# Optimization experiments

Hardware: AMD Instinct MI355X
Metric: run time of the kernel (lower is better)

Reference implementation:

```python
import jax, jax.numpy as jnp
import numpy as np

B, S, D = 2, 2048, 2048
H = 16
KV_RANK = 512
NOPE, ROPE = 128, 64
QK_HD = NOPE + ROPE  # 192
V_HD = 128
SCALE = QK_HD ** -0.5
EPS = 1.1920929e-07  # torch RMSNorm default eps = finfo(fp32).eps
NEG = -1e9


def rmsnorm(x, w):
    return x * jax.lax.rsqrt(jnp.mean(x * x, axis=-1, keepdims=True) + EPS) * w


def apply_rope(x, freqs):
    # x: (b, s, h, r) interleaved pairs; freqs: (s, r//2) angles
    sh = x.shape
    xr = x.reshape(*sh[:-1], -1, 2)
    a, b = xr[..., 0], xr[..., 1]
    cos = jnp.cos(freqs)[None, :, None, :]
    sin = jnp.sin(freqs)[None, :, None, :]
    return jnp.stack([a * cos - b * sin, a * sin + b * cos], axis=-1).reshape(sh)


def setup_inputs() -> dict:
    key = jax.random.key(0)
    ks = jax.random.split(key, 8)
    inv = lambda k, shape, fan_in: jax.random.uniform(k, shape, jnp.float32, -1.0, 1.0) / np.sqrt(fan_in)
    x = jax.random.normal(ks[0], (B, S, D), jnp.float32)
    freqs = jax.random.uniform(ks[1], (S, ROPE // 2), jnp.float32) * np.float32(np.pi)
    mask = jnp.where(jnp.triu(jnp.ones((S, S), bool), k=1), jnp.float32(NEG), jnp.float32(0.0))
    wq_w = inv(ks[2], (H * QK_HD, D), D)
    wq_b = jnp.zeros((H * QK_HD,), jnp.float32)
    wkv_a_w = inv(ks[3], (KV_RANK + ROPE, D), D)
    wkv_a_b = jnp.zeros((KV_RANK + ROPE,), jnp.float32)
    kv_norm_w = jnp.ones((KV_RANK,), jnp.float32)
    wkv_b_w = inv(ks[4], (H * (NOPE + V_HD), KV_RANK), KV_RANK)
    wo_w = inv(ks[5], (D, H * V_HD), H * V_HD)
    wo_b = jnp.zeros((D,), jnp.float32)
    return dict(x=x, freqs=freqs, mask=mask, wq_w=wq_w, wq_b=wq_b,
                wkv_a_w=wkv_a_w, wkv_a_b=wkv_a_b, kv_norm_w=kv_norm_w,
                wkv_b_w=wkv_b_w, wo_w=wo_w, wo_b=wo_b)


def reference(x, freqs, mask, wq_w, wq_b, wkv_a_w, wkv_a_b, kv_norm_w, wkv_b_w, wo_w, wo_b):
    b, s, _ = x.shape
    # q projection (q_lora_rank == 0 path)
    q = (x @ wq_w.T + wq_b).reshape(b, s, H, QK_HD)
    q_nope, q_pe = q[..., :NOPE], q[..., NOPE:]
    q_pe = apply_rope(q_pe, freqs)
    # latent kv projection
    kv = x @ wkv_a_w.T + wkv_a_b
    kv, k_pe = kv[..., :KV_RANK], kv[..., KV_RANK:]
    k_pe = apply_rope(k_pe[:, :, None, :], freqs)[:, :, 0, :]  # (b, t, r)
    kv_proj = rmsnorm(kv, kv_norm_w)  # (b, t, c)
    wkv_b = wkv_b_w.reshape(H, NOPE + V_HD, KV_RANK)
    # absorb K-nope projection into q
    q_nope = jnp.einsum('bshd,hdc->bshc', q_nope, wkv_b[:, :NOPE])
    scores = (jnp.einsum('bshc,btc->bsht', q_nope, kv_proj)
              + jnp.einsum('bshr,btr->bsht', q_pe, k_pe)) * SCALE
    scores = scores + mask[None, :, None, :]
    scores = jax.nn.softmax(scores.astype(jnp.float32), axis=-1).astype(x.dtype)
    out = jnp.einsum('bsht,btc->bshc', scores, kv_proj)
    out = jnp.einsum('bshc,hdc->bshd', out, wkv_b[:, -V_HD:])
    return out.reshape(b, s, H * V_HD) @ wo_w.T + wo_b
```

## Files before the change

kernel.cpp:

```cpp
#include <hip/hip_runtime.h>
#include <hip/hip_bf16.h>
#include <math.h>

#define B_ 2
#define S_ 2048
#define H_ 16
#define SCALE_ 0.07216878364870323f
#define SL2_ (0.07216878364870323f * 1.4426950408889634f)
#define EPS_ 1.1920929e-07f
#define M0_ 8.0f

typedef __attribute__((ext_vector_type(8))) short bf16x8;
typedef __attribute__((ext_vector_type(4))) float f32x4;
union U4 { uint4 u; bf16x8 v; f32x4 f; };

__device__ __forceinline__ uint bfbits(float x) {
    uint u = __float_as_uint(x);
    return (u + 0x7fffu + ((u >> 16) & 1u)) >> 16;
}
__device__ __forceinline__ uint pack2bf(float a, float b) {
    return bfbits(a) | (bfbits(b) << 16);
}
__device__ __forceinline__ uint cvtpk(float a, float b) {
    uint r;
    asm("v_cvt_pk_bf16_f32 %0, %1, %2" : "=v"(r) : "v"(a), "v"(b));
    return r;
}
__device__ __forceinline__ void gld_lds16(const ushort* g, ushort* l) {
    __builtin_amdgcn_global_load_lds(
        (const __attribute__((address_space(1))) uint*)g,
        (__attribute__((address_space(3))) uint*)l, 16, 0, 0);
}

template<bool OUT_BF16>
__global__ __launch_bounds__(256) void mgemm(
    const ushort* __restrict__ A, int lda, long long aOff1, long long aOff2,
    const ushort* __restrict__ Bm, int ldb, long long bOff1, long long bOff2,
    const float* __restrict__ bias, float scale,
    void* __restrict__ Cv, int ldc, long long cOff1, long long cOff2,
    int K, int zDiv)
{
    __shared__ ushort As[128 * 32];
    __shared__ ushort Bs[128 * 32];

    const int z = blockIdx.z;
    const int z1 = z % zDiv, z2 = z / zDiv;
    A  += z1 * aOff1 + z2 * aOff2;
    Bm += z1 * bOff1 + z2 * bOff2;
    const long long cBase = z1 * cOff1 + z2 * cOff2;

    const int n0 = blockIdx.x * 128;
    const int m0 = blockIdx.y * 128;
    const int tid = threadIdx.x;
    const int w   = tid >> 6;
    const int l   = tid & 63;
    const int m   = l & 15;
    const int q4  = l >> 4;
    const int mw  = (w & 1) * 64;
    const int nw  = (w >> 1) * 64;
    const int sr  = l >> 2;
    const int sc  = l & 3;

    f32x4 acc[4][4];
#pragma unroll
    for (int i = 0; i < 4; ++i)
#pragma unroll
        for (int j = 0; j < 4; ++j) acc[i][j] = (f32x4){0.f, 0.f, 0.f, 0.f};

    for (int k0 = 0; k0 < K; k0 += 32) {
#pragma unroll
        for (int jj = 0; jj < 2; ++jj) {
            const int slot = w * 2 + jj;
            const int row  = slot * 16 + sr;
            const int g    = sc ^ ((row >> 1) & 3);
            gld_lds16(&A[(long long)(m0 + row) * lda + k0 + g * 8], &As[slot * 512]);
            gld_lds16(&Bm[(long long)(n0 + row) * ldb + k0 + g * 8], &Bs[slot * 512]);
        }
        __syncthreads();

        U4 af[4], bf[4];
#pragma unroll
        for (int i = 0; i < 4; ++i) {
            const int ra = mw + i * 16 + m;
            af[i].u = *(const uint4*)&As[ra * 32 + (q4 ^ ((ra >> 1) & 3)) * 8];
            const int rb = nw + i * 16 + m;
            bf[i].u = *(const uint4*)&Bs[rb * 32 + (q4 ^ ((rb >> 1) & 3)) * 8];
        }
#pragma unroll
        for (int i = 0; i < 4; ++i)
#pragma unroll
            for (int j = 0; j < 4; ++j)
                acc[i][j] = __builtin_amdgcn_mfma_f32_16x16x32_bf16(
                    af[i].v, bf[j].v, acc[i][j], 0, 0, 0);
        __syncthreads();
    }

#pragma unroll
    for (int j = 0; j < 4; ++j) {
        const int cn = n0 + nw + j * 16 + m;
        const float bv = bias ? bias[cn] : 0.0f;
#pragma unroll
        for (int i = 0; i < 4; ++i) {
            const int rw = m0 + mw + i * 16 + q4 * 4;
#pragma unroll
            for (int r = 0; r < 4; ++r) {
                const float val = acc[i][j][r] * scale + bv;
                if (OUT_BF16)
                    ((ushort*)Cv)[cBase + (long long)(rw + r) * ldc + cn] =
                        (ushort)bfbits(val);
                else
                    ((float*)Cv)[cBase + (long long)(rw + r) * ldc + cn] = val;
            }
        }
    }
}

__global__ __launch_bounds__(256) void conv_all(
    const float* __restrict__ x, const float* __restrict__ wq,
    const float* __restrict__ wkva, const float* __restrict__ wo,
    const float* __restrict__ wkvb,
    ushort* __restrict__ x_bf, ushort* __restrict__ wq_bf,
    ushort* __restrict__ wkva_bf, ushort* __restrict__ wo_bf,
    ushort* __restrict__ wkvbK, ushort* __restrict__ wkvbV)
{
    const int bid = blockIdx.x;
    const int tid = threadIdx.x;
    if (bid < 8192) {
        const long long i = ((long long)bid * 256 + tid) * 4;
        float4 v = *(const float4*)&x[i];
        uint2 p; p.x = pack2bf(v.x, v.y); p.y = pack2bf(v.z, v.w);
        *(uint2*)&x_bf[i] = p;
    } else if (bid < 14336) {
        const long long i = ((long long)(bid - 8192) * 256 + tid) * 4;
        float4 v = *(const float4*)&wq[i];
        uint2 p; p.x = pack2bf(v.x, v.y); p.y = pack2bf(v.z, v.w);
        *(uint2*)&wq_bf[i] = p;
    } else if (bid < 15616) {
        const int i = ((bid - 14336) * 256 + tid) * 4;
        const int r = i >> 11;
        uint2 p = make_uint2(0u, 0u);
        if (r < 576) {
            float4 v = *(const float4*)&wkva[i];
            p.x = pack2bf(v.x, v.y); p.y = pack2bf(v.z, v.w);
        }
        *(uint2*)&wkva_bf[i] = p;
    } else if (bid < 19712) {
        const long long i = ((long long)(bid - 15616) * 256 + tid) * 4;
        float4 v = *(const float4*)&wo[i];
        uint2 p; p.x = pack2bf(v.x, v.y); p.y = pack2bf(v.z, v.w);
        *(uint2*)&wo_bf[i] = p;
    } else if (bid < 20736) {
        const int i = ((bid - 19712) * 256 + tid) * 4;
        const int h = i >> 16, rem = i & 65535;
        float4 v = *(const float4*)&wkvb[((long long)(h * 256)) * 512 + rem];
        uint2 p; p.x = pack2bf(v.x, v.y); p.y = pack2bf(v.z, v.w);
        *(uint2*)&wkvbK[i] = p;
    } else {
        const int i = ((bid - 20736) * 256 + tid) * 4;
        const int h = i >> 16, rem = i & 65535;
        float4 v = *(const float4*)&wkvb[((long long)(h * 256 + 128)) * 512 + rem];
        uint2 p; p.x = pack2bf(v.x, v.y); p.y = pack2bf(v.z, v.w);
        *(uint2*)&wkvbV[i] = p;
    }
}

__global__ __launch_bounds__(256) void qprep(
    const float* __restrict__ q_raw, const float* __restrict__ freqs,
    ushort* __restrict__ q192)
{
    const int idx = blockIdx.x * 256 + threadIdx.x;
    const int row = idx / 48;
    const int c4  = idx % 48;
    const int bs = row >> 4, h = row & 15;
    const float* src = q_raw + (long long)bs * 3072 + h * 192;
    if (c4 < 32) {
        const int d = c4 * 4;
        float4 v = *(const float4*)&src[d];
        uint2 p;
        p.x = pack2bf(v.x * SL2_, v.y * SL2_);
        p.y = pack2bf(v.z * SL2_, v.w * SL2_);
        *(uint2*)&q192[(long long)row * 192 + d] = p;
    } else {
        const int j = c4 - 32;
        const int s = bs & 2047;
        const float f0 = freqs[s * 32 + j * 2];
        const float f1 = freqs[s * 32 + j * 2 + 1];
        float c0, s0, c1, s1;
        __sincosf(f0, &s0, &c0);
        __sincosf(f1, &s1, &c1);
        float4 v = *(const float4*)&src[128 + j * 4];
        uint2 p;
        p.x = pack2bf((v.x * c0 - v.y * s0) * SL2_, (v.x * s0 + v.y * c0) * SL2_);
        p.y = pack2bf((v.z * c1 - v.w * s1) * SL2_, (v.z * s1 + v.w * c1) * SL2_);
        *(uint2*)&q192[(long long)row * 192 + 128 + j * 4] = p;
    }
}

__global__ __launch_bounds__(64) void kv_post_kernel(
    const float* __restrict__ kv_raw, const float* __restrict__ bias,
    const float* __restrict__ w, const float* __restrict__ freqs,
    ushort* __restrict__ kv_h)
{
    const int bs = blockIdx.x;
    const int lane = threadIdx.x;
    const float* src = kv_raw + (long long)bs * 640;
    ushort* dst = kv_h + (long long)bs * 576;

    const int c = 4 * lane;
    float4 v0 = *(const float4*)&src[c];
    float4 v1 = *(const float4*)&src[256 + c];
    float4 b0 = *(const float4*)&bias[c];
    float4 b1 = *(const float4*)&bias[256 + c];
    v0.x += b0.x; v0.y += b0.y; v0.z += b0.z; v0.w += b0.w;
    v1.x += b1.x; v1.y += b1.y; v1.z += b1.z; v1.w += b1.w;
    float ss = v0.x * v0.x + v0.y * v0.y + v0.z * v0.z + v0.w * v0.w +
               v1.x * v1.x + v1.y * v1.y + v1.z * v1.z + v1.w * v1.w;
#pragma unroll
    for (int o = 32; o; o >>= 1) ss += __shfl_xor(ss, o, 64);
    const float rs = rsqrtf(ss * (1.0f / 512.0f) + EPS_);

    float4 w0 = *(const float4*)&w[c];
    float4 w1 = *(const float4*)&w[256 + c];
    uint2 p0, p1;
    p0.x = pack2bf(v0.x * rs * w0.x, v0.y * rs * w0.y);
    p0.y = pack2bf(v0.z * rs * w0.z, v0.w * rs * w0.w);
    p1.x = pack2bf(v1.x * rs * w1.x, v1.y * rs * w1.y);
    p1.y = pack2bf(v1.z * rs * w1.z, v1.w * rs * w1.w);
    *(uint2*)&dst[c] = p0;
    *(uint2*)&dst[256 + c] = p1;

    if (lane < 32) {
        const int s = bs & 2047;
        const float f = freqs[s * 32 + lane];
        float cs, sn;
        __sincosf(f, &sn, &cs);
        const float a  = src[512 + 2 * lane]     + bias[512 + 2 * lane];
        const float b2 = src[512 + 2 * lane + 1] + bias[512 + 2 * lane + 1];
        *(uint*)&dst[512 + 2 * lane] = pack2bf(a * cs - b2 * sn, a * sn + b2 * cs);
    }
}

__global__ __launch_bounds__(256) void prep_all(
    const ushort* __restrict__ K_h, const ushort* __restrict__ V_hT,
    const ushort* __restrict__ kv_h,
    uint4* __restrict__ khimg, uint4* __restrict__ vhimg,
    uint4* __restrict__ rimg)
{
    const int bid = blockIdx.x;
    if (bid < 4096) {
        const int g = bid * 256 + threadIdx.x;
        const int lane = g & 63, ck = (g >> 6) & 7, h = (g >> 9) & 15;
        const int tile = (g >> 13) & 63, b = g >> 19;
        const int m = lane & 15, q4 = lane >> 4, f = ck >> 1, s = ck & 1;
        const uint4 v = *(const uint4*)&K_h[
            ((long long)(b * S_ + tile * 32 + s * 16 + m)) * 2048 + h * 128 + f * 32 + q4 * 8];
        khimg[(((long long)(b * 64 + tile) * 16 + h) * 8 + ck) * 64 + lane] = v;
    } else if (bid < 8192) {
        const int g = (bid - 4096) * 256 + threadIdx.x;
        const int lane = g & 63, c = (g >> 6) & 7, h = (g >> 9) & 15;
        const int tile = (g >> 13) & 63, b = g >> 19;
        const int m = lane & 15, q4 = lane >> 4;
        const uint4 v = *(const uint4*)&V_hT[
            ((long long)((b * 16 + h) * 128 + c * 16 + m)) * 2048 + tile * 32 + q4 * 8];
        vhimg[(((long long)(b * 64 + tile) * 16 + h) * 8 + c) * 64 + lane] = v;
    } else {
        const int g = (bid - 8192) * 256 + threadIdx.x;
        const int lane = g & 63, ck = (g >> 6) & 3, tile = (g >> 8) & 63, b = g >> 14;
        const int m = lane & 15, q4 = lane >> 4, f2 = ck >> 1, s = ck & 1;
        const uint4 v = *(const uint4*)&kv_h[
            ((long long)(b * S_ + tile * 32 + s * 16 + m)) * 576 + 512 + f2 * 32 + q4 * 8];
        rimg[((long long)(b * 64 + tile) * 4 + ck) * 64 + lane] = v;
    }
}

__global__ __launch_bounds__(256, 2) void attn_kernel(
    const ushort* __restrict__ q192,
    const uint4*  __restrict__ khimg,
    const uint4*  __restrict__ rimg,
    const uint4*  __restrict__ vhimg,
    ushort* __restrict__ o_h)
{
    __shared__ uint buf[2][20 * 256];

    const int hb   = blockIdx.x;
    const int h    = hb & 15;
    const int b    = hb >> 4;
    const int chunk = 15 - (int)blockIdx.y;
    const int tid  = threadIdx.x;
    const int wid  = tid >> 6;
    const int lane = tid & 63;
    const int m    = lane & 15;
    const int q4   = lane >> 4;

    const int row0a = chunk * 128 + wid * 16;
    const int row0b = row0a + 64;
    const int sRa   = row0a + m;
    const int sRb   = row0b + m;

    auto stage = [&](int bs, int it) {
        const long long tb = (long long)(b * 64 + it);
        const uint4* kb = khimg + ((tb * 16 + h) * 8) * 64;
        const uint4* rb = rimg  + (tb * 4) * 64;
        const uint4* vb = vhimg + ((tb * 16 + h) * 8) * 64;
        ushort* l = (ushort*)&buf[bs][0];
        gld_lds16((const ushort*)(kb + (wid    ) * 64 + lane), l + (wid     ) * 512);
        gld_lds16((const ushort*)(kb + (wid + 4) * 64 + lane), l + (wid +  4) * 512);
        gld_lds16((const ushort*)(rb + (wid    ) * 64 + lane), l + (wid +  8) * 512);
        gld_lds16((const ushort*)(vb + (wid    ) * 64 + lane), l + (wid + 12) * 512);
        gld_lds16((const ushort*)(vb + (wid + 4) * 64 + lane), l + (wid + 16) * 512);
    };

    U4 qfa[6], qfb[6];
    {
        const uint4* qpa = (const uint4*)(q192 + ((long long)(b * S_ + sRa) * H_ + h) * 192);
        const uint4* qpb = (const uint4*)(q192 + ((long long)(b * S_ + sRb) * H_ + h) * 192);
#pragma unroll
        for (int f = 0; f < 6; ++f) { qfa[f].u = qpa[f * 4 + q4]; qfb[f].u = qpb[f * 4 + q4]; }
    }

    f32x4 oA[8], oB[8];
#pragma unroll
    for (int c = 0; c < 8; ++c) {
        oA[c] = (f32x4){0.f, 0.f, 0.f, 0.f};
        oB[c] = (f32x4){0.f, 0.f, 0.f, 0.f};
    }
    float lA = 0.0f, lB = 0.0f;

    auto softpack = [&](const f32x4 s0, const f32x4 s1, int t0v, int rw0,
                        float& lac) -> U4 {
        float p00, p01, p02, p03, p10, p11, p12, p13;
        if (t0v + 31 <= rw0) {
            p00 = exp2f(s0[0] - M0_); p01 = exp2f(s0[1] - M0_);
            p02 = exp2f(s0[2] - M0_); p03 = exp2f(s0[3] - M0_);
            p10 = exp2f(s1[0] - M0_); p11 = exp2f(s1[1] - M0_);
            p12 = exp2f(s1[2] - M0_); p13 = exp2f(s1[3] - M0_);
        } else {
            const int sR = rw0 + m;
            const int tb0 = t0v + q4 * 4;
            const int tb1 = tb0 + 16;
            p00 = (tb0 + 0 <= sR) ? exp2f(s0[0] - M0_) : 0.0f;
            p01 = (tb0 + 1 <= sR) ? exp2f(s0[1] - M0_) : 0.0f;
            p02 = (tb0 + 2 <= sR) ? exp2f(s0[2] - M0_) : 0.0f;
            p03 = (tb0 + 3 <= sR) ? exp2f(s0[3] - M0_) : 0.0f;
            p10 = (tb1 + 0 <= sR) ? exp2f(s1[0] - M0_) : 0.0f;
            p11 = (tb1 + 1 <= sR) ? exp2f(s1[1] - M0_) : 0.0f;
            p12 = (tb1 + 2 <= sR) ? exp2f(s1[2] - M0_) : 0.0f;
            p13 = (tb1 + 3 <= sR) ? exp2f(s1[3] - M0_) : 0.0f;
        }
        lac += (p00 + p01) + (p02 + p03) + (p10 + p11) + (p12 + p13);
        U4 bb;
        {
            uint pk00 = cvtpk(p00, p01);
            uint pk01 = cvtpk(p02, p03);
            uint pk10 = cvtpk(p10, p11);
            uint pk11 = cvtpk(p12, p13);
            const int srcA = ((lane >> 4) & 1) * 32 + m;
            const int srcB = srcA + 16;
            uint a00 = (uint)__shfl((int)pk00, srcA, 64);
            uint a01 = (uint)__shfl((int)pk01, srcA, 64);
            uint a10 = (uint)__shfl((int)pk10, srcA, 64);
            uint a11 = (uint)__shfl((int)pk11, srcA, 64);
            uint b00 = (uint)__shfl((int)pk00, srcB, 64);
            uint b01 = (uint)__shfl((int)pk01, srcB, 64);
            uint b10 = (uint)__shfl((int)pk10, srcB, 64);
            uint b11 = (uint)__shfl((int)pk11, srcB, 64);
            const bool hi2 = (lane >> 5) & 1;
            bb.u.x = hi2 ? a10 : a00;
            bb.u.y = hi2 ? a11 : a01;
            bb.u.z = hi2 ? b10 : b00;
            bb.u.w = hi2 ? b11 : b01;
        }
        return bb;
    };

    const int nT = chunk * 4 + 4;
    stage(0, 0);
    int cur = 0;

    for (int it = 0; it < nT; ++it) {
        const int t0 = it * 32;
        __syncthreads();
        if (it + 1 < nT) stage(cur ^ 1, it + 1);
        __builtin_amdgcn_sched_barrier(0);

        const uint* bb0 = &buf[cur][0];
        const int abase = lane * 4;
        const bool liveB = (t0 <= row0b + 15);
        const bool liveA = (t0 <= row0a + 15);
        const bool twoA  = (t0 < row0a);
        const bool twoB  = (t0 < row0b);

        if (liveB) {
            f32x4 sA0 = (f32x4){0.f,0.f,0.f,0.f}, sA1 = (f32x4){0.f,0.f,0.f,0.f};
            f32x4 sB0 = (f32x4){0.f,0.f,0.f,0.f}, sB1 = (f32x4){0.f,0.f,0.f,0.f};

            if (twoA) {
#pragma unroll
                for (int f = 0; f < 6; ++f) {
                    const int ck = (f < 4) ? f * 2 : (f - 4) * 2 + 8;
                    U4 a0, a1;
                    a0.u = *(const uint4*)&bb0[ck * 256 + abase];
                    a1.u = *(const uint4*)&bb0[(ck + 1) * 256 + abase];
                    sA0 = __builtin_amdgcn_mfma_f32_16x16x32_bf16(a0.v, qfa[f].v, sA0, 0, 0, 0);
                    sB0 = __builtin_amdgcn_mfma_f32_16x16x32_bf16(a0.v, qfb[f].v, sB0, 0, 0, 0);
                    sA1 = __builtin_amdgcn_mfma_f32_16x16x32_bf16(a1.v, qfa[f].v, sA1, 0, 0, 0);
                    sB1 = __builtin_amdgcn_mfma_f32_16x16x32_bf16(a1.v, qfb[f].v, sB1, 0, 0, 0);
                }
            } else {
#pragma unroll
                for (int f = 0; f < 6; ++f) {
                    const int ck = (f < 4) ? f * 2 : (f - 4) * 2 + 8;
                    U4 a0;
                    a0.u = *(const uint4*)&bb0[ck * 256 + abase];
                    if (liveA)
                        sA0 = __builtin_amdgcn_mfma_f32_16x16x32_bf16(a0.v, qfa[f].v, sA0, 0, 0, 0);
                    sB0 = __builtin_amdgcn_mfma_f32_16x16x32_bf16(a0.v, qfb[f].v, sB0, 0, 0, 0);
                    if (twoB) {
                        U4 a1;
                        a1.u = *(const uint4*)&bb0[(ck + 1) * 256 + abase];
                        sB1 = __builtin_amdgcn_mfma_f32_16x16x32_bf16(a1.v, qfb[f].v, sB1, 0, 0, 0);
                    }
                }
            }

            U4 bbB = softpack(sB0, sB1, t0, row0b, lB);
            if (liveA) {
                U4 bbA = softpack(sA0, sA1, t0, row0a, lA);
#pragma unroll
                for (int c = 0; c < 8; ++c) {
                    U4 av; av.u = *(const uint4*)&bb0[(12 + c) * 256 + abase];
                    oB[c] = __builtin_amdgcn_mfma_f32_16x16x32_bf16(av.v, bbB.v, oB[c], 0, 0, 0);
                    oA[c] = __builtin_amdgcn_mfma_f32_16x16x32_bf16(av.v, bbA.v, oA[c], 0, 0, 0);
                }
            } else {
#pragma unroll
                for (int c = 0; c < 8; ++c) {
                    U4 av; av.u = *(const uint4*)&bb0[(12 + c) * 256 + abase];
                    oB[c] = __builtin_amdgcn_mfma_f32_16x16x32_bf16(av.v, bbB.v, oB[c], 0, 0, 0);
                }
            }
        }
        cur ^= 1;
    }

    lA += __shfl_xor(lA, 16, 64);
    lA += __shfl_xor(lA, 32, 64);
    lB += __shfl_xor(lB, 16, 64);
    lB += __shfl_xor(lB, 32, 64);
    const float invA = 1.0f / lA;
    const float invB = 1.0f / lB;

    ushort* opa = o_h + ((long long)(b * S_ + sRa) * H_ + h) * 128;
    ushort* opb = o_h + ((long long)(b * S_ + sRb) * H_ + h) * 128;
#pragma unroll
    for (int c = 0; c < 8; ++c) {
        uint2 pva, pvb;
        pva.x = cvtpk(oA[c][0] * invA, oA[c][1] * invA);
        pva.y = cvtpk(oA[c][2] * invA, oA[c][3] * invA);
        pvb.x = cvtpk(oB[c][0] * invB, oB[c][1] * invB);
        pvb.y = cvtpk(oB[c][2] * invB, oB[c][3] * invB);
        *(uint2*)&opa[c * 16 + q4 * 4] = pva;
        *(uint2*)&opb[c * 16 + q4 * 4] = pvb;
    }
}

extern "C" void kernel_launch(void* const* d_in, const int* in_sizes, int n_in,
                              void* d_out, int out_size, void* d_ws, size_t ws_size,
                              hipStream_t stream)
{
    const float* x         = (const float*)d_in[0];
    const float* freqs     = (const float*)d_in[1];
    const float* wq_w      = (const float*)d_in[3];
    const float* wq_b      = (const float*)d_in[4];
    const float* wkv_a_w   = (const float*)d_in[5];
    const float* wkv_a_b   = (const float*)d_in[6];
    const float* kv_norm_w = (const float*)d_in[7];
    const float* wkv_b_w   = (const float*)d_in[8];
    const float* wo_w      = (const float*)d_in[9];
    const float* wo_b      = (const float*)d_in[10];
    float* out = (float*)d_out;

    char* w = (char*)d_ws;
    ushort* x_bf    = (ushort*)w;  w += 16777216;
    ushort* wq_bf   = (ushort*)w;  w += 12582912;
    ushort* wkva_bf = (ushort*)w;  w += 2621440;
    ushort* wo_bf   = (ushort*)w;  w += 8388608;
    ushort* wkvbK   = (ushort*)w;  w += 2097152;
    ushort* wkvbV   = (ushort*)w;  w += 2097152;
    float*  kv_raw  = (float*)w;   w += 10485760;
    ushort* kv_h    = (ushort*)w;  w += 4718592;
    ushort* K_h     = (ushort*)w;  w += 16777216;
    ushort* V_hT    = (ushort*)w;  w += 16777216;
    uint4*  khimg   = (uint4*)w;   w += 16777216;
    uint4*  vhimg   = (uint4*)w;   w += 16777216;
    uint4*  rimg    = (uint4*)w;   w += 524288;
    char* RA = w;                  w += 50331648;
    float*  q_raw = (float*)RA;
    ushort* o_h   = (ushort*)RA;
    ushort* q192  = (ushort*)w;    w += 25165824;

    dim3 blk(256);

    conv_all<<<dim3(21760), blk, 0, stream>>>(
        x, wq_w, wkv_a_w, wo_w, wkv_b_w,
        x_bf, wq_bf, wkva_bf, wo_bf, wkvbK, wkvbV);

    mgemm<false><<<dim3(24, 32, 1), blk, 0, stream>>>(
        x_bf, 2048, 0LL, 0LL, wq_bf, 2048, 0LL, 0LL, wq_b, 1.0f,
        q_raw, 3072, 0LL, 0LL, 2048, 1);

    mgemm<false><<<dim3(5, 32, 1), blk, 0, stream>>>(
        x_bf, 2048, 0LL, 0LL, wkva_bf, 2048, 0LL, 0LL, nullptr, 1.0f,
        kv_raw, 640, 0LL, 0LL, 2048, 1);

    qprep<<<dim3(12288), blk, 0, stream>>>(q_raw, freqs, q192);

    kv_post_kernel<<<dim3(4096), dim3(64), 0, stream>>>(
        kv_raw, wkv_a_b, kv_norm_w, freqs, kv_h);

    mgemm<true><<<dim3(1, 16, 32), blk, 0, stream>>>(
        kv_h, 576, 0LL, (long long)S_ * 576,
        wkvbK, 512, 65536LL, 0LL, nullptr, 1.0f,
        K_h, 2048, 128LL, (long long)S_ * 2048, 512, 16);
    mgemm<true><<<dim3(16, 1, 32), blk, 0, stream>>>(
        wkvbV, 512, 65536LL, 0LL,
        kv_h, 576, 0LL, (long long)S_ * 576, nullptr, 1.0f,
        V_hT, 2048, 262144LL, 4194304LL, 512, 16);

    prep_all<<<dim3(8320), blk, 0, stream>>>(K_h, V_hT, kv_h, khimg, vhimg, rimg);

    attn_kernel<<<dim3(32, 16, 1), blk, 0, stream>>>(q192, khimg, rimg, vhimg, o_h);

    mgemm<false><<<dim3(16, 32, 1), blk, 0, stream>>>(
        o_h, 2048, 0LL, 0LL, wo_bf, 2048, 0LL, 0LL, wo_b, 1.0f,
        out, 2048, 0LL, 0LL, 2048, 1);
}
```

Baseline: 491.1 us.

## Pair causal chunks per block for balanced work and use permlane swap

Each attention block now handles two query chunks (p and 15-p) in sequence, so every block does the same amount of causal work, and the grid shrinks from 512 to 256 blocks. The P-matrix repacking in softpack replaces eight cross-lane shuffles with v_permlane32_swap plus ds_swizzle. The intent is to remove the tail imbalance from causal triangles and cut shuffle cost. The trade-off is fewer blocks (256, roughly one per CU) and a serial second pass with no overlap between passes.

```diff
diff --git a/kernel.cpp b/kernel.cpp
--- a/kernel.cpp
+++ b/kernel.cpp
@@ -282,20 +282,15 @@
 {
     __shared__ uint buf[2][20 * 256];
 
-    const int hb   = blockIdx.x;
-    const int h    = hb & 15;
-    const int b    = hb >> 4;
-    const int chunk = 15 - (int)blockIdx.y;
+    const int p    = blockIdx.x;
+    const int h    = blockIdx.y;
+    const int b    = blockIdx.z;
     const int tid  = threadIdx.x;
     const int wid  = tid >> 6;
     const int lane = tid & 63;
     const int m    = lane & 15;
     const int q4   = lane >> 4;
-
-    const int row0a = chunk * 128 + wid * 16;
-    const int row0b = row0a + 64;
-    const int sRa   = row0a + m;
-    const int sRb   = row0b + m;
+    const bool odd = q4 & 1;
 
     auto stage = [&](int bs, int it) {
         const long long tb = (long long)(b * 64 + it);
@@ -310,157 +305,157 @@
         gld_lds16((const ushort*)(vb + (wid + 4) * 64 + lane), l + (wid + 16) * 512);
     };
 
-    U4 qfa[6], qfb[6];
-    {
-        const uint4* qpa = (const uint4*)(q192 + ((long long)(b * S_ + sRa) * H_ + h) * 192);
-        const uint4* qpb = (const uint4*)(q192 + ((long long)(b * S_ + sRb) * H_ + h) * 192);
-#pragma unroll
-        for (int f = 0; f < 6; ++f) { qfa[f].u = qpa[f * 4 + q4]; qfb[f].u = qpb[f * 4 + q4]; }
-    }
-
-    f32x4 oA[8], oB[8];
-#pragma unroll
-    for (int c = 0; c < 8; ++c) {
-        oA[c] = (f32x4){0.f, 0.f, 0.f, 0.f};
-        oB[c] = (f32x4){0.f, 0.f, 0.f, 0.f};
-    }
-    float lA = 0.0f, lB = 0.0f;
-
-    auto softpack = [&](const f32x4 s0, const f32x4 s1, int t0v, int rw0,
-                        float& lac) -> U4 {
-        float p00, p01, p02, p03, p10, p11, p12, p13;
-        if (t0v + 31 <= rw0) {
-            p00 = exp2f(s0[0] - M0_); p01 = exp2f(s0[1] - M0_);
-            p02 = exp2f(s0[2] - M0_); p03 = exp2f(s0[3] - M0_);
-            p10 = exp2f(s1[0] - M0_); p11 = exp2f(s1[1] - M0_);
-            p12 = exp2f(s1[2] - M0_); p13 = exp2f(s1[3] - M0_);
-        } else {
-            const int sR = rw0 + m;
-            const int tb0 = t0v + q4 * 4;
-            const int tb1 = tb0 + 16;
-            p00 = (tb0 + 0 <= sR) ? exp2f(s0[0] - M0_) : 0.0f;
-            p01 = (tb0 + 1 <= sR) ? exp2f(s0[1] - M0_) : 0.0f;
-            p02 = (tb0 + 2 <= sR) ? exp2f(s0[2] - M0_) : 0.0f;
-            p03 = (tb0 + 3 <= sR) ? exp2f(s0[3] - M0_) : 0.0f;
-            p10 = (tb1 + 0 <= sR) ? exp2f(s1[0] - M0_) : 0.0f;
-            p11 = (tb1 + 1 <= sR) ? exp2f(s1[1] - M0_) : 0.0f;
-            p12 = (tb1 + 2 <= sR) ? exp2f(s1[2] - M0_) : 0.0f;
-            p13 = (tb1 + 3 <= sR) ? exp2f(s1[3] - M0_) : 0.0f;
-        }
-        lac += (p00 + p01) + (p02 + p03) + (p10 + p11) + (p12 + p13);
-        U4 bb;
+    int cur = 0;
+    for (int pass = 0; pass < 2; ++pass) {
+        const int chunk = pass ? p : (15 - p);
+        const int row0a = chunk * 128 + wid * 16;
+        const int row0b = row0a + 64;
+        const int sRa   = row0a + m;
+        const int sRb   = row0b + m;
+
+        U4 qfa[6], qfb[6];
         {
-            uint pk00 = cvtpk(p00, p01);
-            uint pk01 = cvtpk(p02, p03);
-            uint pk10 = cvtpk(p10, p11);
-            uint pk11 = cvtpk(p12, p13);
-            const int srcA = ((lane >> 4) & 1) * 32 + m;
-            const int srcB = srcA + 16;
-            uint a00 = (uint)__shfl((int)pk00, srcA, 64);
-            uint a01 = (uint)__shfl((int)pk01, srcA, 64);
-            uint a10 = (uint)__shfl((int)pk10, srcA, 64);
-            uint a11 = (uint)__shfl((int)pk11, srcA, 64);
-            uint b00 = (uint)__shfl((int)pk00, srcB, 64);
-            uint b01 = (uint)__shfl((int)pk01, srcB, 64);
-            uint b10 = (uint)__shfl((int)pk10, srcB, 64);
-            uint b11 = (uint)__shfl((int)pk11, srcB, 64);
-            const bool hi2 = (lane >> 5) & 1;
-            bb.u.x = hi2 ? a10 : a00;
-            bb.u.y = hi2 ? a11 : a01;
-            bb.u.z = hi2 ? b10 : b00;
-            bb.u.w = hi2 ? b11 : b01;
-        }
-        return bb;
-    };
-
-    const int nT = chunk * 4 + 4;
-    stage(0, 0);
-    int cur = 0;
-
-    for (int it = 0; it < nT; ++it) {
-        const int t0 = it * 32;
+            const uint4* qpa = (const uint4*)(q192 + ((long long)(b * S_ + sRa) * H_ + h) * 192);
+            const uint4* qpb = (const uint4*)(q192 + ((long long)(b * S_ + sRb) * H_ + h) * 192);
+#pragma unroll
+            for (int f = 0; f < 6; ++f) { qfa[f].u = qpa[f * 4 + q4]; qfb[f].u = qpb[f * 4 + q4]; }
+        }
+
+        f32x4 oA[8], oB[8];
+#pragma unroll
+        for (int c = 0; c < 8; ++c) {
+            oA[c] = (f32x4){0.f, 0.f, 0.f, 0.f};
+            oB[c] = (f32x4){0.f, 0.f, 0.f, 0.f};
+        }
+        float lA = 0.0f, lB = 0.0f;
+
+        auto softpack = [&](const f32x4 s0, const f32x4 s1, int t0v, int rw0,
+                            float& lac) -> U4 {
+            float p00, p01, p02, p03, p10, p11, p12, p13;
+            if (t0v + 31 <= rw0) {
+                p00 = exp2f(s0[0] - M0_); p01 = exp2f(s0[1] - M0_);
+                p02 = exp2f(s0[2] - M0_); p03 = exp2f(s0[3] - M0_);
+                p10 = exp2f(s1[0] - M0_); p11 = exp2f(s1[1] - M0_);
+                p12 = exp2f(s1[2] - M0_); p13 = exp2f(s1[3] - M0_);
+            } else {
+                const int sR = rw0 + m;
+                const int tb0 = t0v + q4 * 4;
+                const int tb1 = tb0 + 16;
+                p00 = (tb0 + 0 <= sR) ? exp2f(s0[0] - M0_) : 0.0f;
+                p01 = (tb0 + 1 <= sR) ? exp2f(s0[1] - M0_) : 0.0f;
+                p02 = (tb0 + 2 <= sR) ? exp2f(s0[2] - M0_) : 0.0f;
+                p03 = (tb0 + 3 <= sR) ? exp2f(s0[3] - M0_) : 0.0f;
+                p10 = (tb1 + 0 <= sR) ? exp2f(s1[0] - M0_) : 0.0f;
+                p11 = (tb1 + 1 <= sR) ? exp2f(s1[1] - M0_) : 0.0f;
+                p12 = (tb1 + 2 <= sR) ? exp2f(s1[2] - M0_) : 0.0f;
+                p13 = (tb1 + 3 <= sR) ? exp2f(s1[3] - M0_) : 0.0f;
+            }
+            lac += (p00 + p01) + (p02 + p03) + (p10 + p11) + (p12 + p13);
+            uint X0 = cvtpk(p00, p01), X1 = cvtpk(p02, p03);
+            uint Y0 = cvtpk(p10, p11), Y1 = cvtpk(p12, p13);
+            asm("v_permlane32_swap_b32 %0, %1" : "+v"(X0), "+v"(Y0));
+            asm("v_permlane32_swap_b32 %0, %1" : "+v"(X1), "+v"(Y1));
+            uint u0 = odd ? X0 : Y0;
+            uint u1 = odd ? X1 : Y1;
+            uint w0 = (uint)__builtin_amdgcn_ds_swizzle((int)u0, 0x401F);
+            uint w1 = (uint)__builtin_amdgcn_ds_swizzle((int)u1, 0x401F);
+            U4 bb;
+            bb.u.x = odd ? w0 : X0;
+            bb.u.y = odd ? w1 : X1;
+            bb.u.z = odd ? Y0 : w0;
+            bb.u.w = odd ? Y1 : w1;
+            return bb;
+        };
+
+        const int nT = chunk * 4 + 4;
         __syncthreads();
-        if (it + 1 < nT) stage(cur ^ 1, it + 1);
-        __builtin_amdgcn_sched_barrier(0);
-
-        const uint* bb0 = &buf[cur][0];
-        const int abase = lane * 4;
-        const bool liveB = (t0 <= row0b + 15);
-        const bool liveA = (t0 <= row0a + 15);
-        const bool twoA  = (t0 < row0a);
-        const bool twoB  = (t0 < row0b);
-
-        if (liveB) {
-            f32x4 sA0 = (f32x4){0.f,0.f,0.f,0.f}, sA1 = (f32x4){0.f,0.f,0.f,0.f};
-            f32x4 sB0 = (f32x4){0.f,0.f,0.f,0.f}, sB1 = (f32x4){0.f,0.f,0.f,0.f};
-
-            if (twoA) {
-#pragma unroll
-                for (int f = 0; f < 6; ++f) {
-                    const int ck = (f < 4) ? f * 2 : (f - 4) * 2 + 8;
-                    U4 a0, a1;
-                    a0.u = *(const uint4*)&bb0[ck * 256 + abase];
-                    a1.u = *(const uint4*)&bb0[(ck + 1) * 256 + abase];
-                    sA0 = __builtin_amdgcn_mfma_f32_16x16x32_bf16(a0.v, qfa[f].v, sA0, 0, 0, 0);
-                    sB0 = __builtin_amdgcn_mfma_f32_16x16x32_bf16(a0.v, qfb[f].v, sB0, 0, 0, 0);
-                    sA1 = __builtin_amdgcn_mfma_f32_16x16x32_bf16(a1.v, qfa[f].v, sA1, 0, 0, 0);
-                    sB1 = __builtin_amdgcn_mfma_f32_16x16x32_bf16(a1.v, qfb[f].v, sB1, 0, 0, 0);
+        stage(cur, 0);
+
+        for (int it = 0; it < nT; ++it) {
+            const int t0 = it * 32;
+            __syncthreads();
+            if (it + 1 < nT) stage(cur ^ 1, it + 1);
+            __builtin_amdgcn_sched_barrier(0);
+
+            const uint* bb0 = &buf[cur][0];
+            const int abase = lane * 4;
+            const bool liveB = (t0 <= row0b + 15);
+            const bool liveA = (t0 <= row0a + 15);
+            const bool twoA  = (t0 < row0a);
+            const bool twoB  = (t0 < row0b);
+
+            if (liveB) {
+                f32x4 sA0 = (f32x4){0.f,0.f,0.f,0.f}, sA1 = (f32x4){0.f,0.f,0.f,0.f};
+                f32x4 sB0 = (f32x4){0.f,0.f,0.f,0.f}, sB1 = (f32x4){0.f,0.f,0.f,0.f};
+
+                if (twoA) {
+#pragma unroll
+                    for (int f = 0; f < 6; ++f) {
+                        const int ck = (f < 4) ? f * 2 : (f - 4) * 2 + 8;
+                        U4 a0, a1;
+                        a0.u = *(const uint4*)&bb0[ck * 256 + abase];
+                        a1.u = *(const uint4*)&bb0[(ck + 1) * 256 + abase];
+                        sA0 = __builtin_amdgcn_mfma_f32_16x16x32_bf16(a0.v, qfa[f].v, sA0, 0, 0, 0);
+                        sB0 = __builtin_amdgcn_mfma_f32_16x16x32_bf16(a0.v, qfb[f].v, sB0, 0, 0, 0);
+                        sA1 = __builtin_amdgcn_mfma_f32_16x16x32_bf16(a1.v, qfa[f].v, sA1, 0, 0, 0);
+                        sB1 = __builtin_amdgcn_mfma_f32_16x16x32_bf16(a1.v, qfb[f].v, sB1, 0, 0, 0);
+                    }
+                } else {
+#pragma unroll
+                    for (int f = 0; f < 6; ++f) {
+                        const int ck = (f < 4) ? f * 2 : (f - 4) * 2 + 8;
+                        U4 a0;
+                        a0.u = *(const uint4*)&bb0[ck * 256 + abase];
+                        if (liveA)
+                            sA0 = __builtin_amdgcn_mfma_f32_16x16x32_bf16(a0.v, qfa[f].v, sA0, 0, 0, 0);
+                        sB0 = __builtin_amdgcn_mfma_f32_16x16x32_bf16(a0.v, qfb[f].v, sB0, 0, 0, 0);
+                        if (twoB) {
+                            U4 a1;
+                            a1.u = *(const uint4*)&bb0[(ck + 1) * 256 + abase];
+                            sB1 = __builtin_amdgcn_mfma_f32_16x16x32_bf16(a1.v, qfb[f].v, sB1, 0, 0, 0);
+                        }
+                    }
                 }
-            } else {
-#pragma unroll
-                for (int f = 0; f < 6; ++f) {
-                    const int ck = (f < 4) ? f * 2 : (f - 4) * 2 + 8;
-                    U4 a0;
-                    a0.u = *(const uint4*)&bb0[ck * 256 + abase];
-                    if (liveA)
-                        sA0 = __builtin_amdgcn_mfma_f32_16x16x32_bf16(a0.v, qfa[f].v, sA0, 0, 0, 0);
-                    sB0 = __builtin_amdgcn_mfma_f32_16x16x32_bf16(a0.v, qfb[f].v, sB0, 0, 0, 0);
-                    if (twoB) {
-                        U4 a1;
-                        a1.u = *(const uint4*)&bb0[(ck + 1) * 256 + abase];
-                        sB1 = __builtin_amdgcn_mfma_f32_16x16x32_bf16(a1.v, qfb[f].v, sB1, 0, 0, 0);
+
+                U4 bbB = softpack(sB0, sB1, t0, row0b, lB);
+                if (liveA) {
+                    U4 bbA = softpack(sA0, sA1, t0, row0a, lA);
+#pragma unroll
+                    for (int c = 0; c < 8; ++c) {
+                        U4 av; av.u = *(const uint4*)&bb0[(12 + c) * 256 + abase];
+                        oB[c] = __builtin_amdgcn_mfma_f32_16x16x32_bf16(av.v, bbB.v, oB[c], 0, 0, 0);
+                        oA[c] = __builtin_amdgcn_mfma_f32_16x16x32_bf16(av.v, bbA.v, oA[c], 0, 0, 0);
+                    }
+                } else {
+#pragma unroll
+                    for (int c = 0; c < 8; ++c) {
+                        U4 av; av.u = *(const uint4*)&bb0[(12 + c) * 256 + abase];
+                        oB[c] = __builtin_amdgcn_mfma_f32_16x16x32_bf16(av.v, bbB.v, oB[c], 0, 0, 0);
                     }
                 }
             }
-
-            U4 bbB = softpack(sB0, sB1, t0, row0b, lB);
-            if (liveA) {
-                U4 bbA = softpack(sA0, sA1, t0, row0a, lA);
-#pragma unroll
-                for (int c = 0; c < 8; ++c) {
-                    U4 av; av.u = *(const uint4*)&bb0[(12 + c) * 256 + abase];
-                    oB[c] = __builtin_amdgcn_mfma_f32_16x16x32_bf16(av.v, bbB.v, oB[c], 0, 0, 0);
-                    oA[c] = __builtin_amdgcn_mfma_f32_16x16x32_bf16(av.v, bbA.v, oA[c], 0, 0, 0);
-                }
-            } else {
-#pragma unroll
-                for (int c = 0; c < 8; ++c) {
-                    U4 av; av.u = *(const uint4*)&bb0[(12 + c) * 256 + abase];
-                    oB[c] = __builtin_amdgcn_mfma_f32_16x16x32_bf16(av.v, bbB.v, oB[c], 0, 0, 0);
-                }
-            }
-        }
-        cur ^= 1;
-    }
-
-    lA += __shfl_xor(lA, 16, 64);
-    lA += __shfl_xor(lA, 32, 64);
-    lB += __shfl_xor(lB, 16, 64);
-    lB += __shfl_xor(lB, 32, 64);
-    const float invA = 1.0f / lA;
-    const float invB = 1.0f / lB;
-
-    ushort* opa = o_h + ((long long)(b * S_ + sRa) * H_ + h) * 128;
-    ushort* opb = o_h + ((long long)(b * S_ + sRb) * H_ + h) * 128;
-#pragma unroll
-    for (int c = 0; c < 8; ++c) {
-        uint2 pva, pvb;
-        pva.x = cvtpk(oA[c][0] * invA, oA[c][1] * invA);
-        pva.y = cvtpk(oA[c][2] * invA, oA[c][3] * invA);
-        pvb.x = cvtpk(oB[c][0] * invB, oB[c][1] * invB);
-        pvb.y = cvtpk(oB[c][2] * invB, oB[c][3] * invB);
-        *(uint2*)&opa[c * 16 + q4 * 4] = pva;
-        *(uint2*)&opb[c * 16 + q4 * 4] = pvb;
+            cur ^= 1;
+        }
+
+        lA += __shfl_xor(lA, 16, 64);
+        lA += __shfl_xor(lA, 32, 64);
+        lB += __shfl_xor(lB, 16, 64);
+        lB += __shfl_xor(lB, 32, 64);
+        const float invA = 1.0f / lA;
+        const float invB = 1.0f / lB;
+
+        ushort* opa = o_h + ((long long)(b * S_ + sRa) * H_ + h) * 128;
+        ushort* opb = o_h + ((long long)(b * S_ + sRb) * H_ + h) * 128;
+#pragma unroll
+        for (int c = 0; c < 8; ++c) {
+            uint2 pva, pvb;
+            pva.x = cvtpk(oA[c][0] * invA, oA[c][1] * invA);
+            pva.y = cvtpk(oA[c][2] * invA, oA[c][3] * invA);
+            pvb.x = cvtpk(oB[c][0] * invB, oB[c][1] * invB);
+            pvb.y = cvtpk(oB[c][2] * invB, oB[c][3] * invB);
+            *(uint2*)&opa[c * 16 + q4 * 4] = pva;
+            *(uint2*)&opb[c * 16 + q4 * 4] = pvb;
+        }
     }
 }
 
@@ -529,7 +524,7 @@
 
     prep_all<<<dim3(8320), blk, 0, stream>>>(K_h, V_hT, kv_h, khimg, vhimg, rimg);
 
-    attn_kernel<<<dim3(32, 16, 1), blk, 0, stream>>>(q192, khimg, rimg, vhimg, o_h);
+    attn_kernel<<<dim3(8, 16, 2), blk, 0, stream>>>(q192, khimg, rimg, vhimg, o_h);
 
     mgemm<false><<<dim3(16, 32, 1), blk, 0, stream>>>(
         o_h, 2048, 0LL, 0LL, wo_bf, 2048, 0LL, 0LL, wo_b, 1.0f,
```

Result: no change. 483.7 us (-1.5%).
